# Kernel tuning notes

Measured on AMD Instinct MI355X. Metric: run time of the kernel, lower is better.

## Reference

```python
import jax, jax.numpy as jnp
import numpy as np

EMB, HEADS, T_BLK = 1024, 16, 2048
B, T = 2, 2048
HD = EMB // HEADS


def setup_inputs() -> dict:
    key = jax.random.key(0)
    ks = jax.random.split(key, 9)
    s = 1.0 / np.sqrt(EMB)
    return {
        "x": jax.random.normal(ks[0], (B, T, EMB), jnp.float32),
        "Wq": jax.random.normal(ks[1], (EMB, EMB), jnp.float32) * s,
        "bq": jax.random.normal(ks[2], (EMB,), jnp.float32) * s,
        "Wk": jax.random.normal(ks[3], (EMB, EMB), jnp.float32) * s,
        "bk": jax.random.normal(ks[4], (EMB,), jnp.float32) * s,
        "Wv": jax.random.normal(ks[5], (EMB, EMB), jnp.float32) * s,
        "bv": jax.random.normal(ks[6], (EMB,), jnp.float32) * s,
        "Wo": jax.random.normal(ks[7], (EMB, EMB), jnp.float32) * s,
        "bo": jax.random.normal(ks[8], (EMB,), jnp.float32) * s,
    }


def reference(x, Wq, bq, Wk, bk, Wv, bv, Wo, bo):
    # eval mode: dropout is identity
    Bn, Tn, C = x.shape
    def proj(W, b):
        y = x @ W.T + b                      # [B,T,C]
        return y.reshape(Bn, Tn, HEADS, HD).transpose(0, 2, 1, 3)  # [B,H,T,hd]
    q, k, v = proj(Wq, bq), proj(Wk, bk), proj(Wv, bv)
    scores = jnp.einsum('bhqd,bhkd->bhqk', q, k) * (HD ** -0.5)  # [B,H,T,T]
    causal = jnp.tril(jnp.ones((Tn, Tn), dtype=bool))
    scores = jnp.where(causal, scores, -jnp.inf)
    w = jax.nn.softmax(scores, axis=-1)
    out = jnp.einsum('bhqk,bhkd->bhqd', w, v)                    # [B,H,T,hd]
    out = out.transpose(0, 2, 1, 3).reshape(Bn, Tn, C)
    return out @ Wo.T + bo
```

## Files before the change

### kernel.cpp

```cpp
#include <hip/hip_runtime.h>
#include <stdint.h>

#define EMB   1024
#define HEADS 16
#define HD    64
#define BB    2
#define TT    2048
#define MTOT  (BB*TT)
#define LDA   72

#define ELX (4194304u)
#define ELW (1048576u)

#define CSCALE (0.125f * 1.44269504088896f)

typedef __attribute__((ext_vector_type(8))) short short8;
typedef __attribute__((ext_vector_type(4))) float f32x4;
typedef __attribute__((ext_vector_type(4))) unsigned short us4;

__device__ __forceinline__ float bf2f(ushort u) {
  union { uint32_t u; float f; } x; x.u = ((uint32_t)u) << 16; return x.f;
}
__device__ __forceinline__ ushort f2bf(float f) {
  union { float f; uint32_t u; } x; x.f = f;
  uint32_t u = x.u;
  u += 0x7fffu + ((u >> 16) & 1u);
  return (ushort)(u >> 16);
}
__device__ __forceinline__ ushort f2bf_trunc(float f) {
  union { float f; uint32_t u; } x; x.f = f;
  return (ushort)(x.u >> 16);
}
__device__ __forceinline__ uint32_t pack2(uint32_t lo, uint32_t hi) {
  return (lo >> 16) | (hi & 0xFFFF0000u);
}
__device__ __forceinline__ short8 pack8(f32x4 a, f32x4 b) {
  union { f32x4 v; uint32_t u[4]; } A, B;
  A.v = a; B.v = b;
  union { uint32_t d[4]; short8 s; } R;
  R.d[0] = pack2(A.u[0], A.u[1]);
  R.d[1] = pack2(A.u[2], A.u[3]);
  R.d[2] = pack2(B.u[0], B.u[1]);
  R.d[3] = pack2(B.u[2], B.u[3]);
  return R.s;
}

__device__ __forceinline__ short8 cvt8_rne(const float* f) {
  f32x4 a = *(const f32x4*)f;
  f32x4 b = *(const f32x4*)(f + 4);
  short8 r;
  r[0] = (short)f2bf(a[0]); r[1] = (short)f2bf(a[1]);
  r[2] = (short)f2bf(a[2]); r[3] = (short)f2bf(a[3]);
  r[4] = (short)f2bf(b[0]); r[5] = (short)f2bf(b[1]);
  r[6] = (short)f2bf(b[2]); r[7] = (short)f2bf(b[3]);
  return r;
}

__global__ void detect_dtype(const uint32_t* __restrict__ x, int* __restrict__ flag) {
  if (threadIdx.x == 0) {
    int cnt = 0;
    for (int i = 0; i < 256; ++i) {
      uint32_t lo = x[i] & 0xFFFFu;
      uint32_t e = (lo >> 7) & 0xFFu;
      if (e >= 0x70u && e <= 0x8Fu) ++cnt;
    }
    *flag = (cnt > 128) ? 1 : 0;
  }
}

__global__ __launch_bounds__(256) void convert3(const void* __restrict__ w0,
                                                const void* __restrict__ w1,
                                                const void* __restrict__ w2,
                                                ushort* __restrict__ dst,
                                                const int* __restrict__ flag) {
  const size_t i = ((size_t)blockIdx.x * 256 + threadIdx.x) * 8;
  const int wi = (int)(i >> 20);
  const size_t off = i & (ELW - 1);
  const void* src = (wi == 0) ? w0 : (wi == 1) ? w1 : w2;
  if (*flag) *(short8*)(dst + i) = *(const short8*)((const ushort*)src + off);
  else       *(short8*)(dst + i) = cvt8_rne((const float*)src + off);
}

template<bool BF> struct PF {
  short8 b0, b1;
  f32x4 f0, f1, f2, f3;
  __device__ __forceinline__ void load(const void* base, size_t i0, size_t i1) {
    if constexpr (BF) {
      b0 = *(const short8*)((const ushort*)base + i0);
      b1 = *(const short8*)((const ushort*)base + i1);
    } else {
      const float* p0 = (const float*)base + i0;
      const float* p1 = (const float*)base + i1;
      f0 = *(const f32x4*)p0; f1 = *(const f32x4*)(p0 + 4);
      f2 = *(const f32x4*)p1; f3 = *(const f32x4*)(p1 + 4);
    }
  }
  __device__ __forceinline__ void store(ushort* l0, ushort* l1) {
    if constexpr (BF) { *(short8*)l0 = b0; *(short8*)l1 = b1; }
    else { *(short8*)l0 = pack8(f0, f1); *(short8*)l1 = pack8(f2, f3); }
  }
};

template<bool ABF, bool WBF>
__device__ __forceinline__ void gemm_pipe128(const void* __restrict__ Ap,
                                             const void* __restrict__ Bp,
                                             int m0, int n0,
                                             ushort* As, ushort* Ws,
                                             f32x4 acc[4][4]) {
  const int tid  = threadIdx.x;
  const int w    = tid >> 6;
  const int lane = tid & 63;
  const int quad = lane >> 4;
  const int l16  = lane & 15;
  const int wrow = w >> 1, wcol = w & 1;
  const int srow = tid >> 2;
  const int scol = (tid & 3) * 8;

  const size_t a0 = (size_t)(m0 + srow) * EMB + scol;
  const size_t a1 = (size_t)(m0 + srow + 64) * EMB + scol;
  const size_t b0 = (size_t)(n0 + srow) * EMB + scol;
  const size_t b1 = (size_t)(n0 + srow + 64) * EMB + scol;

  PF<ABF> pa; PF<WBF> pb;
  pa.load(Ap, a0, a1);
  pb.load(Bp, b0, b1);

  for (int k0 = 0; k0 < EMB; k0 += 32) {
    __syncthreads();
    pa.store(&As[srow * 32 + scol], &As[(srow + 64) * 32 + scol]);
    pb.store(&Ws[srow * 32 + scol], &Ws[(srow + 64) * 32 + scol]);
    if (k0 + 32 < EMB) {
      pa.load(Ap, a0 + k0 + 32, a1 + k0 + 32);
      pb.load(Bp, b0 + k0 + 32, b1 + k0 + 32);
    }
    __syncthreads();

    short8 af[4], bfr[4];
#pragma unroll
    for (int i = 0; i < 4; ++i)
      af[i]  = *(const short8*)&As[(wrow * 64 + i * 16 + l16) * 32 + quad * 8];
#pragma unroll
    for (int i = 0; i < 4; ++i)
      bfr[i] = *(const short8*)&Ws[(wcol * 64 + i * 16 + l16) * 32 + quad * 8];
#pragma unroll
    for (int mi = 0; mi < 4; ++mi)
#pragma unroll
      for (int ni = 0; ni < 4; ++ni)
        acc[mi][ni] = __builtin_amdgcn_mfma_f32_16x16x32_bf16(af[mi], bfr[ni], acc[mi][ni], 0, 0, 0);
  }
}

__device__ __forceinline__ void qkv_epilogue(f32x4 acc[4][4], int mt, int n0, int mat,
                                             const void* bias, int isbf,
                                             ushort* qo, ushort* ko, ushort* vo) {
  const int tid  = threadIdx.x;
  const int w    = tid >> 6;
  const int lane = tid & 63;
  const int quad = lane >> 4;
  const int l16  = lane & 15;
  const int wrow = w >> 1, wcol = w & 1;
  ushort* dst = (mat == 0) ? qo : ko;
  const float sc = (mat == 0) ? CSCALE : 1.0f;

#pragma unroll
  for (int ni = 0; ni < 4; ++ni) {
    const int n = n0 + wcol * 64 + ni * 16 + l16;
    const float bv_ = isbf ? bf2f(((const ushort*)bias)[n]) : ((const float*)bias)[n];
    const int hh = n >> 6, d = n & 63;
#pragma unroll
    for (int mi = 0; mi < 4; ++mi) {
      const int mbase = mt * 128 + wrow * 64 + mi * 16 + quad * 4;
      const int b = mbase >> 11, t = mbase & (TT - 1);
      if (mat == 2) {
        us4 pk;
#pragma unroll
        for (int r = 0; r < 4; ++r) pk[r] = f2bf(acc[mi][ni][r] + bv_);
        *(us4*)&vo[((size_t)((b * HEADS + hh) * HD + d)) * TT + t] = pk;
      } else {
#pragma unroll
        for (int r = 0; r < 4; ++r)
          dst[((size_t)((b * HEADS + hh) * TT + t + r)) * HD + d] = f2bf((acc[mi][ni][r] + bv_) * sc);
      }
    }
  }
}

__global__ __launch_bounds__(256) void qkv_pipe(const void* __restrict__ x,
                                                const ushort* __restrict__ w3,
                                                const void* __restrict__ bq,
                                                const void* __restrict__ bk,
                                                const void* __restrict__ bv,
                                                ushort* __restrict__ qo,
                                                ushort* __restrict__ ko,
                                                ushort* __restrict__ vo,
                                                const int* __restrict__ flag) {
  __shared__ __align__(16) ushort As[128 * 32];
  __shared__ __align__(16) ushort Ws[128 * 32];
  const int nt = blockIdx.x % 24;
  const int mt = blockIdx.x / 24;
  const int mat = nt >> 3;
  const int n0  = (nt & 7) * 128;
  const ushort* W  = w3 + (size_t)mat * ELW;
  const void* bias = (mat == 0) ? bq : (mat == 1) ? bk : bv;

  f32x4 acc[4][4];
#pragma unroll
  for (int i = 0; i < 4; ++i)
#pragma unroll
    for (int j = 0; j < 4; ++j) acc[i][j] = (f32x4){0.f, 0.f, 0.f, 0.f};

  const int isbf = *flag;
  if (isbf) gemm_pipe128<true,  true>(x, W, mt * 128, n0, As, Ws, acc);
  else      gemm_pipe128<false, true>(x, W, mt * 128, n0, As, Ws, acc);
  qkv_epilogue(acc, mt, n0, mat, bias, isbf, qo, ko, vo);
}

__global__ __launch_bounds__(256) void attn3(const ushort* __restrict__ qw,
                                             const ushort* __restrict__ kw,
                                             const ushort* __restrict__ vtw,
                                             ushort* __restrict__ out) {
  __shared__ __align__(16) ushort Ks[64 * LDA];
  __shared__ __align__(16) ushort Vts[64 * LDA];
  __shared__ __align__(16) ushort Ps[4][16 * LDA];

  const int bid = blockIdx.x;
  const int j  = bid >> 8;
  const int r8 = bid & 255;
  const int qh = r8 & 31;
  const int bh = j * 8 + (r8 >> 5);
  int qt;
  if      (j == 0) qt = qh;
  else if (j == 1) qt = 31 - qh;
  else if (j == 2) qt = (qh + 16) & 31;
  else             qt = 31 - ((qh + 16) & 31);
  const int h = bh & (HEADS - 1);
  const int b = bh >> 4;

  const int tid  = threadIdx.x;
  const int w    = tid >> 6;
  const int lane = tid & 63;
  const int quad = lane >> 4;
  const int l16  = lane & 15;

  const size_t hoff = ((size_t)(b * HEADS + h)) * TT * HD;
  const ushort* Qg = qw + hoff;
  const ushort* Kg = kw + hoff;
  const ushort* Vg = vtw + hoff;
  const int q0 = qt * 64;

  short8 qf[2];
  {
    const ushort* qrow = Qg + (size_t)(q0 + w * 16 + l16) * HD;
    qf[0] = *(const short8*)(qrow + quad * 8);
    qf[1] = *(const short8*)(qrow + 32 + quad * 8);
  }

  const int row = tid >> 2;
  const int c0  = (tid & 3) * 16;
  const ushort* Kbase = Kg + (size_t)row * HD + c0;
  const ushort* Vbase = Vg + (size_t)row * TT + c0;

  short8 pk0 = *(const short8*)(Kbase);
  short8 pk1 = *(const short8*)(Kbase + 8);
  short8 pv0 = *(const short8*)(Vbase);
  short8 pv1 = *(const short8*)(Vbase + 8);

  float ls[4] = {0.f, 0.f, 0.f, 0.f};
  f32x4 O[4];
#pragma unroll
  for (int ni = 0; ni < 4; ++ni) O[ni] = (f32x4){0.f, 0.f, 0.f, 0.f};

  for (int kt = 0; kt <= qt; ++kt) {
    const int k0 = kt * 64;
    __syncthreads();
    *(short8*)&Ks[row * LDA + c0]      = pk0;
    *(short8*)&Ks[row * LDA + c0 + 8]  = pk1;
    *(short8*)&Vts[row * LDA + c0]     = pv0;
    *(short8*)&Vts[row * LDA + c0 + 8] = pv1;
    if (kt < qt) {
      const size_t ko_ = (size_t)(k0 + 64) * HD;
      pk0 = *(const short8*)(Kbase + ko_);
      pk1 = *(const short8*)(Kbase + ko_ + 8);
      pv0 = *(const short8*)(Vbase + k0 + 64);
      pv1 = *(const short8*)(Vbase + k0 + 64 + 8);
    }
    __syncthreads();

    f32x4 s[4];
#pragma unroll
    for (int ni = 0; ni < 4; ++ni) s[ni] = (f32x4){0.f, 0.f, 0.f, 0.f};
#pragma unroll
    for (int ks = 0; ks < 2; ++ks) {
#pragma unroll
      for (int ni = 0; ni < 4; ++ni) {
        short8 kb = *(const short8*)&Ks[(ni * 16 + l16) * LDA + ks * 32 + quad * 8];
        s[ni] = __builtin_amdgcn_mfma_f32_16x16x32_bf16(qf[ks], kb, s[ni], 0, 0, 0);
      }
    }

    if (kt == qt) {
#pragma unroll
      for (int ni = 0; ni < 4; ++ni) {
        const int kk = k0 + ni * 16 + l16;
#pragma unroll
        for (int r = 0; r < 4; ++r) {
          const int qq = q0 + w * 16 + quad * 4 + r;
          if (kk > qq) s[ni][r] = -__builtin_inff();
        }
      }
    }

#pragma unroll
    for (int ni = 0; ni < 4; ++ni)
#pragma unroll
      for (int r = 0; r < 4; ++r) {
        const float p = exp2f(s[ni][r]);
        s[ni][r] = p;
        ls[r] += p;
      }

#pragma unroll
    for (int ni = 0; ni < 4; ++ni)
#pragma unroll
      for (int r = 0; r < 4; ++r)
        Ps[w][(quad * 4 + r) * LDA + ni * 16 + l16] = f2bf_trunc(s[ni][r]);

#pragma unroll
    for (int ks = 0; ks < 2; ++ks) {
      short8 a = *(const short8*)&Ps[w][l16 * LDA + ks * 32 + quad * 8];
#pragma unroll
      for (int ni = 0; ni < 4; ++ni) {
        short8 vb = *(const short8*)&Vts[(ni * 16 + l16) * LDA + ks * 32 + quad * 8];
        O[ni] = __builtin_amdgcn_mfma_f32_16x16x32_bf16(a, vb, O[ni], 0, 0, 0);
      }
    }
  }

#pragma unroll
  for (int r = 0; r < 4; ++r) {
#pragma unroll
    for (int off = 1; off < 16; off <<= 1) ls[r] += __shfl_xor(ls[r], off);
    const float inv = 1.0f / ls[r];
    const int t = q0 + w * 16 + quad * 4 + r;
#pragma unroll
    for (int ni = 0; ni < 4; ++ni) {
      out[((size_t)(b * TT + t)) * EMB + h * HD + ni * 16 + l16] = f2bf(O[ni][r] * inv);
    }
  }
}

template<bool WBF>
__device__ __forceinline__ void proj_core(const ushort* __restrict__ A,
                                          const void* __restrict__ Wo,
                                          int m0, int n0,
                                          ushort* As, ushort* Ws,
                                          f32x4 acc[4][2]) {
  const int tid  = threadIdx.x;
  const int w    = tid >> 6;
  const int lane = tid & 63;
  const int quad = lane >> 4;
  const int l16  = lane & 15;
  const int srow = tid >> 2;
  const int scol = (tid & 3) * 8;

  const size_t ai = (size_t)(m0 + srow) * EMB + scol;
  const size_t b0 = (size_t)(n0 + srow) * EMB + scol;
  const size_t b1 = (size_t)(n0 + srow + 64) * EMB + scol;

  short8 pa;
  PF<WBF> pb;
  pa = *(const short8*)(A + ai);
  pb.load(Wo, b0, b1);

  for (int k0 = 0; k0 < EMB; k0 += 32) {
    __syncthreads();
    *(short8*)&As[srow * 32 + scol] = pa;
    pb.store(&Ws[srow * 32 + scol], &Ws[(srow + 64) * 32 + scol]);
    if (k0 + 32 < EMB) {
      pa = *(const short8*)(A + ai + k0 + 32);
      pb.load(Wo, b0 + k0 + 32, b1 + k0 + 32);
    }
    __syncthreads();

    short8 af[4], bfr[2];
#pragma unroll
    for (int i = 0; i < 4; ++i)
      af[i]  = *(const short8*)&As[(i * 16 + l16) * 32 + quad * 8];
#pragma unroll
    for (int i = 0; i < 2; ++i)
      bfr[i] = *(const short8*)&Ws[(w * 32 + i * 16 + l16) * 32 + quad * 8];
#pragma unroll
    for (int mi = 0; mi < 4; ++mi)
#pragma unroll
      for (int ni = 0; ni < 2; ++ni)
        acc[mi][ni] = __builtin_amdgcn_mfma_f32_16x16x32_bf16(af[mi], bfr[ni], acc[mi][ni], 0, 0, 0);
  }
}

__global__ __launch_bounds__(256) void proj_pipe(const ushort* __restrict__ A,
                                                 const void* __restrict__ Wo,
                                                 const void* __restrict__ bo,
                                                 void* __restrict__ out,
                                                 const int* __restrict__ flag) {
  __shared__ __align__(16) ushort As[64 * 32];
  __shared__ __align__(16) ushort Ws[128 * 32];
  const int nt = blockIdx.x & 7;
  const int mt = blockIdx.x >> 3;
  const int n0 = nt * 128;
  const int m0 = mt * 64;

  f32x4 acc[4][2];
#pragma unroll
  for (int i = 0; i < 4; ++i)
#pragma unroll
    for (int jj = 0; jj < 2; ++jj) acc[i][jj] = (f32x4){0.f, 0.f, 0.f, 0.f};

  const int isbf = *flag;
  if (isbf) proj_core<true >(A, Wo, m0, n0, As, Ws, acc);
  else      proj_core<false>(A, Wo, m0, n0, As, Ws, acc);

  const int tid  = threadIdx.x;
  const int w    = tid >> 6;
  const int lane = tid & 63;
  const int quad = lane >> 4;
  const int l16  = lane & 15;

#pragma unroll
  for (int ni = 0; ni < 2; ++ni) {
    const int n = n0 + w * 32 + ni * 16 + l16;
    const float bv_ = isbf ? bf2f(((const ushort*)bo)[n]) : ((const float*)bo)[n];
#pragma unroll
    for (int mi = 0; mi < 4; ++mi) {
#pragma unroll
      for (int r = 0; r < 4; ++r) {
        const int m = m0 + mi * 16 + quad * 4 + r;
        const float v = acc[mi][ni][r] + bv_;
        if (isbf) ((ushort*)out)[(size_t)m * EMB + n] = f2bf(v);
        else      ((float*) out)[(size_t)m * EMB + n] = v;
      }
    }
  }
}

extern "C" void kernel_launch(void* const* d_in, const int* in_sizes, int n_in,
                              void* d_out, int out_size, void* d_ws, size_t ws_size,
                              hipStream_t stream) {
  const void* x  = d_in[0];
  const void* Wq = d_in[1];
  const void* bq = d_in[2];
  const void* Wk = d_in[3];
  const void* bk = d_in[4];
  const void* Wv = d_in[5];
  const void* bv = d_in[6];
  const void* Wo = d_in[7];
  const void* bo = d_in[8];

  int* flag = (int*)d_ws;
  ushort* base = (ushort*)((char*)d_ws + 256);

  ushort* q_ws  = base;
  ushort* k_ws  = q_ws + ELX;
  ushort* vt_ws = k_ws + ELX;
  ushort* w3    = vt_ws + ELX;
  ushort* o_ws  = vt_ws + ELX;

  detect_dtype<<<dim3(1), dim3(64), 0, stream>>>((const uint32_t*)x, flag);
  convert3<<<dim3(1536), dim3(256), 0, stream>>>(Wq, Wk, Wv, w3, flag);
  qkv_pipe<<<dim3(768), dim3(256), 0, stream>>>(x, w3, bq, bk, bv,
                                                q_ws, k_ws, vt_ws, flag);
  attn3<<<dim3(1024), dim3(256), 0, stream>>>(q_ws, k_ws, vt_ws, o_ws);
  proj_pipe<<<dim3(512), dim3(256), 0, stream>>>(o_ws, Wo, bo, d_out, flag);
}
```

Measured before the change: 227.8 us.

## Rework attention into split-K warps and deepen GEMM K-tiles with XCD-aware block mapping

The attention kernel now gives each warp a strided subset of key tiles for all 64 query rows. K and V are read straight from global memory instead of being staged in shared memory, and the partial outputs and row sums are reduced across warps through LDS at the end. The QKV and output-projection GEMMs move to 64-wide K steps with padded LDS rows to cut barrier count and bank conflicts. Block indices are remapped so neighbouring M tiles share an XCD, aiming at better L2 reuse. Risks include higher register pressure, uncached global K/V loads, and load imbalance across warps on short causal rows.

```diff
diff --git a/kernel.cpp b/kernel.cpp
--- a/kernel.cpp
+++ b/kernel.cpp
@@ -7,7 +7,7 @@
 #define BB    2
 #define TT    2048
 #define MTOT  (BB*TT)
-#define LDA   72
+#define LDP   72
 
 #define ELX (4194304u)
 #define ELW (1048576u)
@@ -44,7 +44,6 @@
   R.d[3] = pack2(B.u[2], B.u[3]);
   return R.s;
 }
-
 __device__ __forceinline__ short8 cvt8_rne(const float* f) {
   f32x4 a = *(const f32x4*)f;
   f32x4 b = *(const f32x4*)(f + 4);
@@ -81,72 +80,79 @@
   else       *(short8*)(dst + i) = cvt8_rne((const float*)src + off);
 }
 
-template<bool BF> struct PF {
-  short8 b0, b1;
-  f32x4 f0, f1, f2, f3;
-  __device__ __forceinline__ void load(const void* base, size_t i0, size_t i1) {
-    if constexpr (BF) {
-      b0 = *(const short8*)((const ushort*)base + i0);
-      b1 = *(const short8*)((const ushort*)base + i1);
-    } else {
-      const float* p0 = (const float*)base + i0;
-      const float* p1 = (const float*)base + i1;
-      f0 = *(const f32x4*)p0; f1 = *(const f32x4*)(p0 + 4);
-      f2 = *(const f32x4*)p1; f3 = *(const f32x4*)(p1 + 4);
-    }
-  }
-  __device__ __forceinline__ void store(ushort* l0, ushort* l1) {
-    if constexpr (BF) { *(short8*)l0 = b0; *(short8*)l1 = b1; }
-    else { *(short8*)l0 = pack8(f0, f1); *(short8*)l1 = pack8(f2, f3); }
-  }
-};
-
-template<bool ABF, bool WBF>
-__device__ __forceinline__ void gemm_pipe128(const void* __restrict__ Ap,
-                                             const void* __restrict__ Bp,
-                                             int m0, int n0,
-                                             ushort* As, ushort* Ws,
-                                             f32x4 acc[4][4]) {
+template<bool ABF>
+__device__ __forceinline__ void gemm_qkv(const void* __restrict__ Ap,
+                                         const ushort* __restrict__ Wp,
+                                         int m0, int n0,
+                                         ushort* As, ushort* Ws,
+                                         f32x4 acc[4][4]) {
   const int tid  = threadIdx.x;
   const int w    = tid >> 6;
   const int lane = tid & 63;
   const int quad = lane >> 4;
   const int l16  = lane & 15;
   const int wrow = w >> 1, wcol = w & 1;
-  const int srow = tid >> 2;
-  const int scol = (tid & 3) * 8;
-
-  const size_t a0 = (size_t)(m0 + srow) * EMB + scol;
-  const size_t a1 = (size_t)(m0 + srow + 64) * EMB + scol;
-  const size_t b0 = (size_t)(n0 + srow) * EMB + scol;
-  const size_t b1 = (size_t)(n0 + srow + 64) * EMB + scol;
-
-  PF<ABF> pa; PF<WBF> pb;
-  pa.load(Ap, a0, a1);
-  pb.load(Bp, b0, b1);
-
-  for (int k0 = 0; k0 < EMB; k0 += 32) {
+  const int srow = tid >> 1;
+  const int scol = (tid & 1) * 32;
+
+  const size_t aoff = (size_t)(m0 + srow) * EMB + scol;
+  const size_t boff = (size_t)(n0 + srow) * EMB + scol;
+
+  short8 wa[4];
+  short8 ab[4];
+  f32x4  af8[8];
+  if constexpr (ABF) {
+#pragma unroll
+    for (int i = 0; i < 4; ++i) ab[i] = *(const short8*)((const ushort*)Ap + aoff + 8 * i);
+  } else {
+#pragma unroll
+    for (int i = 0; i < 8; ++i) af8[i] = *(const f32x4*)((const float*)Ap + aoff + 4 * i);
+  }
+#pragma unroll
+  for (int i = 0; i < 4; ++i) wa[i] = *(const short8*)(Wp + boff + 8 * i);
+
+  for (int k0 = 0; k0 < EMB; k0 += 64) {
     __syncthreads();
-    pa.store(&As[srow * 32 + scol], &As[(srow + 64) * 32 + scol]);
-    pb.store(&Ws[srow * 32 + scol], &Ws[(srow + 64) * 32 + scol]);
-    if (k0 + 32 < EMB) {
-      pa.load(Ap, a0 + k0 + 32, a1 + k0 + 32);
-      pb.load(Bp, b0 + k0 + 32, b1 + k0 + 32);
+    if constexpr (ABF) {
+#pragma unroll
+      for (int i = 0; i < 4; ++i) *(short8*)&As[srow * LDP + scol + 8 * i] = ab[i];
+    } else {
+#pragma unroll
+      for (int i = 0; i < 4; ++i)
+        *(short8*)&As[srow * LDP + scol + 8 * i] = pack8(af8[2 * i], af8[2 * i + 1]);
+    }
+#pragma unroll
+    for (int i = 0; i < 4; ++i) *(short8*)&Ws[srow * LDP + scol + 8 * i] = wa[i];
+    if (k0 + 64 < EMB) {
+      if constexpr (ABF) {
+#pragma unroll
+        for (int i = 0; i < 4; ++i)
+          ab[i] = *(const short8*)((const ushort*)Ap + aoff + k0 + 64 + 8 * i);
+      } else {
+#pragma unroll
+        for (int i = 0; i < 8; ++i)
+          af8[i] = *(const f32x4*)((const float*)Ap + aoff + k0 + 64 + 4 * i);
+      }
+#pragma unroll
+      for (int i = 0; i < 4; ++i) wa[i] = *(const short8*)(Wp + boff + k0 + 64 + 8 * i);
     }
     __syncthreads();
 
-    short8 af[4], bfr[4];
-#pragma unroll
-    for (int i = 0; i < 4; ++i)
-      af[i]  = *(const short8*)&As[(wrow * 64 + i * 16 + l16) * 32 + quad * 8];
-#pragma unroll
-    for (int i = 0; i < 4; ++i)
-      bfr[i] = *(const short8*)&Ws[(wcol * 64 + i * 16 + l16) * 32 + quad * 8];
-#pragma unroll
-    for (int mi = 0; mi < 4; ++mi)
-#pragma unroll
-      for (int ni = 0; ni < 4; ++ni)
-        acc[mi][ni] = __builtin_amdgcn_mfma_f32_16x16x32_bf16(af[mi], bfr[ni], acc[mi][ni], 0, 0, 0);
+#pragma unroll
+    for (int ks = 0; ks < 2; ++ks) {
+      short8 af[4], bfr[4];
+#pragma unroll
+      for (int i = 0; i < 4; ++i)
+        af[i]  = *(const short8*)&As[(wrow * 64 + i * 16 + l16) * LDP + ks * 32 + quad * 8];
+#pragma unroll
+      for (int i = 0; i < 4; ++i)
+        bfr[i] = *(const short8*)&Ws[(wcol * 64 + i * 16 + l16) * LDP + ks * 32 + quad * 8];
+#pragma unroll
+      for (int mi = 0; mi < 4; ++mi)
+#pragma unroll
+        for (int ni = 0; ni < 4; ++ni)
+          acc[mi][ni] = __builtin_amdgcn_mfma_f32_16x16x32_bf16(af[mi], bfr[ni], acc[mi][ni], 0, 0, 0);
+    }
   }
 }
 
@@ -194,10 +200,12 @@
                                                 ushort* __restrict__ ko,
                                                 ushort* __restrict__ vo,
                                                 const int* __restrict__ flag) {
-  __shared__ __align__(16) ushort As[128 * 32];
-  __shared__ __align__(16) ushort Ws[128 * 32];
-  const int nt = blockIdx.x % 24;
-  const int mt = blockIdx.x / 24;
+  __shared__ __align__(16) ushort As[128 * LDP];
+  __shared__ __align__(16) ushort Ws[128 * LDP];
+  const int xcd = blockIdx.x & 7;
+  const int i   = blockIdx.x >> 3;
+  const int mt  = xcd * 4 + i / 24;
+  const int nt  = i % 24;
   const int mat = nt >> 3;
   const int n0  = (nt & 7) * 128;
   const ushort* W  = w3 + (size_t)mat * ELW;
@@ -205,23 +213,22 @@
 
   f32x4 acc[4][4];
 #pragma unroll
-  for (int i = 0; i < 4; ++i)
-#pragma unroll
-    for (int j = 0; j < 4; ++j) acc[i][j] = (f32x4){0.f, 0.f, 0.f, 0.f};
+  for (int a = 0; a < 4; ++a)
+#pragma unroll
+    for (int b = 0; b < 4; ++b) acc[a][b] = (f32x4){0.f, 0.f, 0.f, 0.f};
 
   const int isbf = *flag;
-  if (isbf) gemm_pipe128<true,  true>(x, W, mt * 128, n0, As, Ws, acc);
-  else      gemm_pipe128<false, true>(x, W, mt * 128, n0, As, Ws, acc);
+  if (isbf) gemm_qkv<true >(x, W, mt * 128, n0, As, Ws, acc);
+  else      gemm_qkv<false>(x, W, mt * 128, n0, As, Ws, acc);
   qkv_epilogue(acc, mt, n0, mat, bias, isbf, qo, ko, vo);
 }
 
-__global__ __launch_bounds__(256) void attn3(const ushort* __restrict__ qw,
+__global__ __launch_bounds__(256) void attn4(const ushort* __restrict__ qw,
                                              const ushort* __restrict__ kw,
                                              const ushort* __restrict__ vtw,
                                              ushort* __restrict__ out) {
-  __shared__ __align__(16) ushort Ks[64 * LDA];
-  __shared__ __align__(16) ushort Vts[64 * LDA];
-  __shared__ __align__(16) ushort Ps[4][16 * LDA];
+  __shared__ __align__(16) ushort Pbuf[4][64 * LDP];
+  __shared__ float lsA[64], lsB[64];
 
   const int bid = blockIdx.x;
   const int j  = bid >> 8;
@@ -247,105 +254,152 @@
   const ushort* Kg = kw + hoff;
   const ushort* Vg = vtw + hoff;
   const int q0 = qt * 64;
-
-  short8 qf[2];
+  ushort* Pw = &Pbuf[w][0];
+
+  short8 qa[4][2];
+#pragma unroll
+  for (int mi = 0; mi < 4; ++mi) {
+    const ushort* qrow = Qg + (size_t)(q0 + mi * 16 + l16) * HD + quad * 8;
+    qa[mi][0] = *(const short8*)(qrow);
+    qa[mi][1] = *(const short8*)(qrow + 32);
+  }
+
+  f32x4 o[4][4];
+  float ls[4][4];
+#pragma unroll
+  for (int mi = 0; mi < 4; ++mi) {
+#pragma unroll
+    for (int ni = 0; ni < 4; ++ni) o[mi][ni] = (f32x4){0.f, 0.f, 0.f, 0.f};
+#pragma unroll
+    for (int r = 0; r < 4; ++r) ls[mi][r] = 0.f;
+  }
+
+  for (int kt = w; kt <= qt; kt += 4) {
+    const int k0 = kt * 64;
+
+    f32x4 s[4][4];
+#pragma unroll
+    for (int mi = 0; mi < 4; ++mi)
+#pragma unroll
+      for (int ni = 0; ni < 4; ++ni) s[mi][ni] = (f32x4){0.f, 0.f, 0.f, 0.f};
+#pragma unroll
+    for (int ks = 0; ks < 2; ++ks) {
+#pragma unroll
+      for (int ni = 0; ni < 4; ++ni) {
+        short8 kb = *(const short8*)(Kg + (size_t)(k0 + ni * 16 + l16) * HD + ks * 32 + quad * 8);
+#pragma unroll
+        for (int mi = 0; mi < 4; ++mi)
+          s[mi][ni] = __builtin_amdgcn_mfma_f32_16x16x32_bf16(qa[mi][ks], kb, s[mi][ni], 0, 0, 0);
+      }
+    }
+
+    if (kt == qt) {
+#pragma unroll
+      for (int ni = 0; ni < 4; ++ni) {
+        const int kk = ni * 16 + l16;
+#pragma unroll
+        for (int mi = 0; mi < 4; ++mi)
+#pragma unroll
+          for (int r = 0; r < 4; ++r)
+            if (kk > mi * 16 + quad * 4 + r) s[mi][ni][r] = -__builtin_inff();
+      }
+    }
+
+#pragma unroll
+    for (int mi = 0; mi < 4; ++mi)
+#pragma unroll
+      for (int ni = 0; ni < 4; ++ni)
+#pragma unroll
+        for (int r = 0; r < 4; ++r) {
+          const float p = exp2f(s[mi][ni][r]);
+          ls[mi][r] += p;
+          Pw[(mi * 16 + quad * 4 + r) * LDP + ni * 16 + l16] = f2bf_trunc(p);
+        }
+
+#pragma unroll
+    for (int ks = 0; ks < 2; ++ks) {
+      short8 pa[4];
+#pragma unroll
+      for (int mi = 0; mi < 4; ++mi)
+        pa[mi] = *(const short8*)&Pw[(mi * 16 + l16) * LDP + ks * 32 + quad * 8];
+#pragma unroll
+      for (int ni = 0; ni < 4; ++ni) {
+        short8 vb = *(const short8*)(Vg + (size_t)(ni * 16 + l16) * TT + k0 + ks * 32 + quad * 8);
+#pragma unroll
+        for (int mi = 0; mi < 4; ++mi)
+          o[mi][ni] = __builtin_amdgcn_mfma_f32_16x16x32_bf16(pa[mi], vb, o[mi][ni], 0, 0, 0);
+      }
+    }
+  }
+
+  float* bufA = (float*)&Pbuf[0][0];
+  float* bufB = (float*)&Pbuf[2][0];
+
+  __syncthreads();
+  if (w < 2) {
+    float* buf = w ? bufB : bufA;
+#pragma unroll
+    for (int mi = 0; mi < 4; ++mi)
+#pragma unroll
+      for (int ni = 0; ni < 4; ++ni)
+#pragma unroll
+        for (int r = 0; r < 4; ++r)
+          buf[(mi * 16 + quad * 4 + r) * 68 + ni * 16 + l16] = o[mi][ni][r];
+#pragma unroll
+    for (int mi = 0; mi < 4; ++mi)
+#pragma unroll
+      for (int r = 0; r < 4; ++r) {
+#pragma unroll
+        for (int off = 1; off < 16; off <<= 1) ls[mi][r] += __shfl_xor(ls[mi][r], off);
+      }
+    if (l16 == 0) {
+      float* lsp = w ? lsB : lsA;
+#pragma unroll
+      for (int mi = 0; mi < 4; ++mi)
+#pragma unroll
+        for (int r = 0; r < 4; ++r) lsp[mi * 16 + quad * 4 + r] = ls[mi][r];
+    }
+  }
+  __syncthreads();
+  if (w >= 2) {
+    float* buf = (w == 2) ? bufA : bufB;
+#pragma unroll
+    for (int mi = 0; mi < 4; ++mi)
+#pragma unroll
+      for (int ni = 0; ni < 4; ++ni)
+#pragma unroll
+        for (int r = 0; r < 4; ++r)
+          buf[(mi * 16 + quad * 4 + r) * 68 + ni * 16 + l16] += o[mi][ni][r];
+#pragma unroll
+    for (int mi = 0; mi < 4; ++mi)
+#pragma unroll
+      for (int r = 0; r < 4; ++r) {
+#pragma unroll
+        for (int off = 1; off < 16; off <<= 1) ls[mi][r] += __shfl_xor(ls[mi][r], off);
+      }
+    if (l16 == 0) {
+      float* lsp = (w == 2) ? lsA : lsB;
+#pragma unroll
+      for (int mi = 0; mi < 4; ++mi)
+#pragma unroll
+        for (int r = 0; r < 4; ++r) lsp[mi * 16 + quad * 4 + r] += ls[mi][r];
+    }
+  }
+  __syncthreads();
+
   {
-    const ushort* qrow = Qg + (size_t)(q0 + w * 16 + l16) * HD;
-    qf[0] = *(const short8*)(qrow + quad * 8);
-    qf[1] = *(const short8*)(qrow + 32 + quad * 8);
-  }
-
-  const int row = tid >> 2;
-  const int c0  = (tid & 3) * 16;
-  const ushort* Kbase = Kg + (size_t)row * HD + c0;
-  const ushort* Vbase = Vg + (size_t)row * TT + c0;
-
-  short8 pk0 = *(const short8*)(Kbase);
-  short8 pk1 = *(const short8*)(Kbase + 8);
-  short8 pv0 = *(const short8*)(Vbase);
-  short8 pv1 = *(const short8*)(Vbase + 8);
-
-  float ls[4] = {0.f, 0.f, 0.f, 0.f};
-  f32x4 O[4];
-#pragma unroll
-  for (int ni = 0; ni < 4; ++ni) O[ni] = (f32x4){0.f, 0.f, 0.f, 0.f};
-
-  for (int kt = 0; kt <= qt; ++kt) {
-    const int k0 = kt * 64;
-    __syncthreads();
-    *(short8*)&Ks[row * LDA + c0]      = pk0;
-    *(short8*)&Ks[row * LDA + c0 + 8]  = pk1;
-    *(short8*)&Vts[row * LDA + c0]     = pv0;
-    *(short8*)&Vts[row * LDA + c0 + 8] = pv1;
-    if (kt < qt) {
-      const size_t ko_ = (size_t)(k0 + 64) * HD;
-      pk0 = *(const short8*)(Kbase + ko_);
-      pk1 = *(const short8*)(Kbase + ko_ + 8);
-      pv0 = *(const short8*)(Vbase + k0 + 64);
-      pv1 = *(const short8*)(Vbase + k0 + 64 + 8);
-    }
-    __syncthreads();
-
-    f32x4 s[4];
-#pragma unroll
-    for (int ni = 0; ni < 4; ++ni) s[ni] = (f32x4){0.f, 0.f, 0.f, 0.f};
-#pragma unroll
-    for (int ks = 0; ks < 2; ++ks) {
-#pragma unroll
-      for (int ni = 0; ni < 4; ++ni) {
-        short8 kb = *(const short8*)&Ks[(ni * 16 + l16) * LDA + ks * 32 + quad * 8];
-        s[ni] = __builtin_amdgcn_mfma_f32_16x16x32_bf16(qf[ks], kb, s[ni], 0, 0, 0);
-      }
-    }
-
-    if (kt == qt) {
-#pragma unroll
-      for (int ni = 0; ni < 4; ++ni) {
-        const int kk = k0 + ni * 16 + l16;
-#pragma unroll
-        for (int r = 0; r < 4; ++r) {
-          const int qq = q0 + w * 16 + quad * 4 + r;
-          if (kk > qq) s[ni][r] = -__builtin_inff();
-        }
-      }
-    }
-
-#pragma unroll
-    for (int ni = 0; ni < 4; ++ni)
-#pragma unroll
-      for (int r = 0; r < 4; ++r) {
-        const float p = exp2f(s[ni][r]);
-        s[ni][r] = p;
-        ls[r] += p;
-      }
-
-#pragma unroll
-    for (int ni = 0; ni < 4; ++ni)
-#pragma unroll
-      for (int r = 0; r < 4; ++r)
-        Ps[w][(quad * 4 + r) * LDA + ni * 16 + l16] = f2bf_trunc(s[ni][r]);
-
-#pragma unroll
-    for (int ks = 0; ks < 2; ++ks) {
-      short8 a = *(const short8*)&Ps[w][l16 * LDA + ks * 32 + quad * 8];
-#pragma unroll
-      for (int ni = 0; ni < 4; ++ni) {
-        short8 vb = *(const short8*)&Vts[(ni * 16 + l16) * LDA + ks * 32 + quad * 8];
-        O[ni] = __builtin_amdgcn_mfma_f32_16x16x32_bf16(a, vb, O[ni], 0, 0, 0);
-      }
-    }
-  }
-
-#pragma unroll
-  for (int r = 0; r < 4; ++r) {
-#pragma unroll
-    for (int off = 1; off < 16; off <<= 1) ls[r] += __shfl_xor(ls[r], off);
-    const float inv = 1.0f / ls[r];
-    const int t = q0 + w * 16 + quad * 4 + r;
-#pragma unroll
-    for (int ni = 0; ni < 4; ++ni) {
-      out[((size_t)(b * TT + t)) * EMB + h * HD + ni * 16 + l16] = f2bf(O[ni][r] * inv);
-    }
+    const int row = tid >> 2;
+    const int c0  = (tid & 3) * 16;
+    const float inv = 1.0f / (lsA[row] + lsB[row]);
+    short8 o0, o1;
+#pragma unroll
+    for (int k = 0; k < 8; ++k) {
+      o0[k] = (short)f2bf((bufA[row * 68 + c0 + k]     + bufB[row * 68 + c0 + k])     * inv);
+      o1[k] = (short)f2bf((bufA[row * 68 + c0 + 8 + k] + bufB[row * 68 + c0 + 8 + k]) * inv);
+    }
+    ushort* op = &out[((size_t)(b * TT + q0 + row)) * EMB + h * HD + c0];
+    *(short8*)op = o0;
+    *(short8*)(op + 8) = o1;
   }
 }
 
@@ -360,40 +414,69 @@
   const int lane = tid & 63;
   const int quad = lane >> 4;
   const int l16  = lane & 15;
-  const int srow = tid >> 2;
-  const int scol = (tid & 3) * 8;
-
-  const size_t ai = (size_t)(m0 + srow) * EMB + scol;
-  const size_t b0 = (size_t)(n0 + srow) * EMB + scol;
-  const size_t b1 = (size_t)(n0 + srow + 64) * EMB + scol;
-
-  short8 pa;
-  PF<WBF> pb;
-  pa = *(const short8*)(A + ai);
-  pb.load(Wo, b0, b1);
-
-  for (int k0 = 0; k0 < EMB; k0 += 32) {
+  const int arow = tid >> 2;
+  const int acol = (tid & 3) * 16;
+  const int wrw  = tid >> 1;
+  const int wcl  = (tid & 1) * 32;
+
+  const size_t aoff = (size_t)(m0 + arow) * EMB + acol;
+  const size_t boff = (size_t)(n0 + wrw) * EMB + wcl;
+
+  short8 pa2[2];
+  short8 wb[4];
+  f32x4  wf8[8];
+  pa2[0] = *(const short8*)(A + aoff);
+  pa2[1] = *(const short8*)(A + aoff + 8);
+  if constexpr (WBF) {
+#pragma unroll
+    for (int i = 0; i < 4; ++i) wb[i] = *(const short8*)((const ushort*)Wo + boff + 8 * i);
+  } else {
+#pragma unroll
+    for (int i = 0; i < 8; ++i) wf8[i] = *(const f32x4*)((const float*)Wo + boff + 4 * i);
+  }
+
+  for (int k0 = 0; k0 < EMB; k0 += 64) {
     __syncthreads();
-    *(short8*)&As[srow * 32 + scol] = pa;
-    pb.store(&Ws[srow * 32 + scol], &Ws[(srow + 64) * 32 + scol]);
-    if (k0 + 32 < EMB) {
-      pa = *(const short8*)(A + ai + k0 + 32);
-      pb.load(Wo, b0 + k0 + 32, b1 + k0 + 32);
+    *(short8*)&As[arow * LDP + acol]     = pa2[0];
+    *(short8*)&As[arow * LDP + acol + 8] = pa2[1];
+    if constexpr (WBF) {
+#pragma unroll
+      for (int i = 0; i < 4; ++i) *(short8*)&Ws[wrw * LDP + wcl + 8 * i] = wb[i];
+    } else {
+#pragma unroll
+      for (int i = 0; i < 4; ++i)
+        *(short8*)&Ws[wrw * LDP + wcl + 8 * i] = pack8(wf8[2 * i], wf8[2 * i + 1]);
+    }
+    if (k0 + 64 < EMB) {
+      pa2[0] = *(const short8*)(A + aoff + k0 + 64);
+      pa2[1] = *(const short8*)(A + aoff + k0 + 64 + 8);
+      if constexpr (WBF) {
+#pragma unroll
+        for (int i = 0; i < 4; ++i)
+          wb[i] = *(const short8*)((const ushort*)Wo + boff + k0 + 64 + 8 * i);
+      } else {
+#pragma unroll
+        for (int i = 0; i < 8; ++i)
+          wf8[i] = *(const f32x4*)((const float*)Wo + boff + k0 + 64 + 4 * i);
+      }
     }
     __syncthreads();
 
-    short8 af[4], bfr[2];
-#pragma unroll
-    for (int i = 0; i < 4; ++i)
-      af[i]  = *(const short8*)&As[(i * 16 + l16) * 32 + quad * 8];
-#pragma unroll
-    for (int i = 0; i < 2; ++i)
-      bfr[i] = *(const short8*)&Ws[(w * 32 + i * 16 + l16) * 32 + quad * 8];
-#pragma unroll
-    for (int mi = 0; mi < 4; ++mi)
-#pragma unroll
-      for (int ni = 0; ni < 2; ++ni)
-        acc[mi][ni] = __builtin_amdgcn_mfma_f32_16x16x32_bf16(af[mi], bfr[ni], acc[mi][ni], 0, 0, 0);
+#pragma unroll
+    for (int ks = 0; ks < 2; ++ks) {
+      short8 af[4], bfr[2];
+#pragma unroll
+      for (int i = 0; i < 4; ++i)
+        af[i]  = *(const short8*)&As[(i * 16 + l16) * LDP + ks * 32 + quad * 8];
+#pragma unroll
+      for (int i = 0; i < 2; ++i)
+        bfr[i] = *(const short8*)&Ws[(w * 32 + i * 16 + l16) * LDP + ks * 32 + quad * 8];
+#pragma unroll
+      for (int mi = 0; mi < 4; ++mi)
+#pragma unroll
+        for (int ni = 0; ni < 2; ++ni)
+          acc[mi][ni] = __builtin_amdgcn_mfma_f32_16x16x32_bf16(af[mi], bfr[ni], acc[mi][ni], 0, 0, 0);
+    }
   }
 }
 
@@ -402,18 +485,20 @@
                                                  const void* __restrict__ bo,
                                                  void* __restrict__ out,
                                                  const int* __restrict__ flag) {
-  __shared__ __align__(16) ushort As[64 * 32];
-  __shared__ __align__(16) ushort Ws[128 * 32];
-  const int nt = blockIdx.x & 7;
-  const int mt = blockIdx.x >> 3;
-  const int n0 = nt * 128;
-  const int m0 = mt * 64;
+  __shared__ __align__(16) ushort As[64 * LDP];
+  __shared__ __align__(16) ushort Ws[128 * LDP];
+  const int xcd = blockIdx.x & 7;
+  const int i   = blockIdx.x >> 3;
+  const int mt  = xcd * 8 + (i >> 3);
+  const int nt  = i & 7;
+  const int n0  = nt * 128;
+  const int m0  = mt * 64;
 
   f32x4 acc[4][2];
 #pragma unroll
-  for (int i = 0; i < 4; ++i)
-#pragma unroll
-    for (int jj = 0; jj < 2; ++jj) acc[i][jj] = (f32x4){0.f, 0.f, 0.f, 0.f};
+  for (int a = 0; a < 4; ++a)
+#pragma unroll
+    for (int b = 0; b < 2; ++b) acc[a][b] = (f32x4){0.f, 0.f, 0.f, 0.f};
 
   const int isbf = *flag;
   if (isbf) proj_core<true >(A, Wo, m0, n0, As, Ws, acc);
@@ -468,6 +553,6 @@
   convert3<<<dim3(1536), dim3(256), 0, stream>>>(Wq, Wk, Wv, w3, flag);
   qkv_pipe<<<dim3(768), dim3(256), 0, stream>>>(x, w3, bq, bk, bv,
                                                 q_ws, k_ws, vt_ws, flag);
-  attn3<<<dim3(1024), dim3(256), 0, stream>>>(q_ws, k_ws, vt_ws, o_ws);
+  attn4<<<dim3(1024), dim3(256), 0, stream>>>(q_ws, k_ws, vt_ws, o_ws);
   proj_pipe<<<dim3(512), dim3(256), 0, stream>>>(o_ws, Wo, bo, d_out, flag);
 }
```

Measured after the change: 359.9 us. +57.9%, slower.
